# Performance work log

Hardware: AMD Instinct MI355X
Metric: run time of the kernel (lower is better)

Reference implementation:

```python
import jax, jax.numpy as jnp
import numpy as np

N_EMBD = 1024
N_HEAD = 16
HEAD_DIM = N_EMBD // N_HEAD
B, T = 2, 2048


def setup_inputs() -> dict:
    key = jax.random.key(0)
    ks = jax.random.split(key, 12)
    s = 0.02
    inp = {
        "x": jax.random.normal(ks[0], (B, T, N_EMBD), dtype=jnp.float32),
        "ln1_g": jnp.ones((N_EMBD,), jnp.float32),
        "ln1_b": jnp.zeros((N_EMBD,), jnp.float32),
        "ln2_g": jnp.ones((N_EMBD,), jnp.float32),
        "ln2_b": jnp.zeros((N_EMBD,), jnp.float32),
        "W_qkv": jax.random.normal(ks[1], (N_EMBD, 3 * N_EMBD), jnp.float32) * s,
        "b_qkv": jnp.zeros((3 * N_EMBD,), jnp.float32),
        "W_o": jax.random.normal(ks[2], (N_EMBD, N_EMBD), jnp.float32) * s,
        "b_o": jnp.zeros((N_EMBD,), jnp.float32),
        "W_fc": jax.random.normal(ks[3], (N_EMBD, 4 * N_EMBD), jnp.float32) * s,
        "b_fc": jnp.zeros((4 * N_EMBD,), jnp.float32),
        "W_proj": jax.random.normal(ks[4], (4 * N_EMBD, N_EMBD), jnp.float32) * s,
        "b_proj": jnp.zeros((N_EMBD,), jnp.float32),
    }
    return inp


def _layernorm(x, g, b, eps=1e-5):
    mu = jnp.mean(x, axis=-1, keepdims=True)
    var = jnp.var(x, axis=-1, keepdims=True)
    return (x - mu) * jax.lax.rsqrt(var + eps) * g + b


def _block(x, ln1_g, ln1_b, ln2_g, ln2_b, W_qkv, b_qkv, W_o, b_o, W_fc, b_fc, W_proj, b_proj):
    # --- attention sub-block (pre-LN) ---
    h = _layernorm(x, ln1_g, ln1_b)
    qkv = h @ W_qkv + b_qkv                     # [B,T,3E]
    q, k, v = jnp.split(qkv, 3, axis=-1)
    def split_heads(t):
        return t.reshape(B, T, N_HEAD, HEAD_DIM).transpose(0, 2, 1, 3)  # [B,H,T,D]
    q, k, v = split_heads(q), split_heads(k), split_heads(v)
    scores = jnp.einsum("bhqd,bhkd->bhqk", q, k) / (HEAD_DIM ** 0.5)
    causal = jnp.tril(jnp.ones((T, T), dtype=bool))
    scores = jnp.where(causal, scores, jnp.float32(-jnp.inf))
    probs = jax.nn.softmax(scores, axis=-1)
    attn = jnp.einsum("bhqk,bhkd->bhqd", probs, v)        # [B,H,T,D]
    attn = attn.transpose(0, 2, 1, 3).reshape(B, T, N_EMBD)
    x = x + attn @ W_o + b_o
    # --- MLP sub-block (pre-LN) ---
    h = _layernorm(x, ln2_g, ln2_b)
    h = jax.nn.gelu(h @ W_fc + b_fc, approximate=False)
    x = x + h @ W_proj + b_proj
    return x


def reference(x, ln1_g, ln1_b, ln2_g, ln2_b, W_qkv, b_qkv, W_o, b_o, W_fc, b_fc, W_proj, b_proj):
    return _block(x, ln1_g, ln1_b, ln2_g, ln2_b, W_qkv, b_qkv, W_o, b_o, W_fc, b_fc, W_proj, b_proj)
```

## Files before the change

kernel.cpp:

```cpp
#include <hip/hip_runtime.h>
#include <hip/hip_bf16.h>


#define TT 2048
#define EE 1024
#define NH 16
#define HD 64

#define AS1 __attribute__((address_space(1)))
#define AS3 __attribute__((address_space(3)))

using bf16x8 = __bf16 __attribute__((ext_vector_type(8)));
using bf16x4 = __bf16 __attribute__((ext_vector_type(4)));
using f32x4  = float __attribute__((ext_vector_type(4)));

__global__ __launch_bounds__(256) void convt_kernel(const float* __restrict__ W,
                                                    __bf16* __restrict__ WT,
                                                    int K, int N) {
    __shared__ __bf16 t[32][33];
    int n0 = blockIdx.x * 32, k0 = blockIdx.y * 32;
    int tid = threadIdx.x;
    int r = tid >> 3, c4 = (tid & 7) * 4;
    float4 v = *(const float4*)(W + (size_t)(k0 + r) * N + n0 + c4);
    t[r][c4 + 0] = (__bf16)v.x; t[r][c4 + 1] = (__bf16)v.y;
    t[r][c4 + 2] = (__bf16)v.z; t[r][c4 + 3] = (__bf16)v.w;
    __syncthreads();
    bf16x4 o;
    o[0] = t[c4 + 0][r]; o[1] = t[c4 + 1][r];
    o[2] = t[c4 + 2][r]; o[3] = t[c4 + 3][r];
    *(bf16x4*)(WT + (size_t)(n0 + r) * K + k0 + c4) = o;
}

__global__ __launch_bounds__(256) void ln_kernel(const float* __restrict__ x,
                                                 const float* __restrict__ g,
                                                 const float* __restrict__ bta,
                                                 __bf16* __restrict__ out) {
    int row = blockIdx.x;
    int tid = threadIdx.x;
    const float4 xv = *(const float4*)(x + (size_t)row * EE + tid * 4);
    float s  = xv.x + xv.y + xv.z + xv.w;
    float ss = xv.x*xv.x + xv.y*xv.y + xv.z*xv.z + xv.w*xv.w;
    __shared__ float rs[256], rss[256];
    rs[tid] = s; rss[tid] = ss;
    __syncthreads();
    for (int st = 128; st > 0; st >>= 1) {
        if (tid < st) { rs[tid] += rs[tid+st]; rss[tid] += rss[tid+st]; }
        __syncthreads();
    }
    float mean = rs[0] * (1.0f / EE);
    float var  = rss[0] * (1.0f / EE) - mean * mean;
    float rstd = rsqrtf(var + 1e-5f);
    const float4 gv = *(const float4*)(g + tid * 4);
    const float4 bv = *(const float4*)(bta + tid * 4);
    bf16x4 ov;
    ov[0] = (__bf16)((xv.x - mean) * rstd * gv.x + bv.x);
    ov[1] = (__bf16)((xv.y - mean) * rstd * gv.y + bv.y);
    ov[2] = (__bf16)((xv.z - mean) * rstd * gv.z + bv.z);
    ov[3] = (__bf16)((xv.w - mean) * rstd * gv.w + bv.w);
    *(bf16x4*)(out + (size_t)row * EE + tid * 4) = ov;
}

template<int TM, int TN, bool GELU, bool RESID, bool QKV, typename CT>
__global__ __launch_bounds__(256) void gemm_bt_kernel(const __bf16* __restrict__ A,
                                                      const __bf16* __restrict__ BT,
                                                      const float* __restrict__ bias,
                                                      const float* resid, CT* C,
                                                      __bf16* vT,
                                                      int M, int N, int K) {
    constexpr int MT = TM / 32;
    constexpr int NT = TN / 32;
    __shared__ __align__(16) __bf16 As[TM][32];
    __shared__ __align__(16) __bf16 Bs[TN][32];
    int tid = threadIdx.x, wave = tid >> 6, lane = tid & 63;
    int quad = lane >> 4, l16 = lane & 15;
    int wm = wave >> 1, wn = wave & 1;
    int m0 = blockIdx.y * TM, n0 = blockIdx.x * TN;

    f32x4 acc[MT][NT] = {};

    int srow = wave * 16 + (lane >> 2);
    int scol = (lane & 3) * 8;

    for (int kb = 0; kb < K; kb += 32) {
#pragma unroll
        for (int p = 0; p < TM / 64; p++) {
            const __bf16* g = A + (size_t)(m0 + p * 64 + srow) * K + kb + scol;
            __builtin_amdgcn_global_load_lds((AS1 const void*)g,
                                             (AS3 void*)&As[p * 64 + wave * 16][0], 16, 0, 0);
        }
#pragma unroll
        for (int p = 0; p < TN / 64; p++) {
            const __bf16* g = BT + (size_t)(n0 + p * 64 + srow) * K + kb + scol;
            __builtin_amdgcn_global_load_lds((AS1 const void*)g,
                                             (AS3 void*)&Bs[p * 64 + wave * 16][0], 16, 0, 0);
        }
        __syncthreads();
        bf16x8 af[MT], bfr[NT];
#pragma unroll
        for (int mt = 0; mt < MT; mt++)
            af[mt] = *(const bf16x8*)(&As[wm * (MT * 16) + mt * 16 + l16][quad * 8]);
#pragma unroll
        for (int nt = 0; nt < NT; nt++)
            bfr[nt] = *(const bf16x8*)(&Bs[wn * (NT * 16) + nt * 16 + l16][quad * 8]);
#pragma unroll
        for (int mt = 0; mt < MT; mt++)
#pragma unroll
            for (int nt = 0; nt < NT; nt++)
                acc[mt][nt] = __builtin_amdgcn_mfma_f32_16x16x32_bf16(af[mt], bfr[nt],
                                                                      acc[mt][nt], 0, 0, 0);
        __syncthreads();
    }

#pragma unroll
    for (int nt = 0; nt < NT; nt++) {
        int c = n0 + wn * (NT * 16) + nt * 16 + l16;
        float bv = bias[c];
#pragma unroll
        for (int mt = 0; mt < MT; mt++) {
#pragma unroll
            for (int r = 0; r < 4; r++) {
                int row = m0 + wm * (MT * 16) + mt * 16 + quad * 4 + r;
                float v = acc[mt][nt][r] + bv;
                if (GELU)  v = 0.5f * v * (1.0f + erff(v * 0.70710678118f));
                if (RESID) v += resid[(size_t)row * N + c];
                if (!QKV) {
                    C[(size_t)row * N + c] = (CT)v;
                } else {
                    if (c < 2 * EE) {
                        ((__bf16*)C)[(size_t)row * (2 * EE) + c] = (__bf16)v;
                    } else {
                        int cv = c - 2 * EE;
                        int bb = row >> 11, t = row & (TT - 1);
                        vT[((size_t)(bb * NH + (cv >> 6)) * HD + (cv & 63)) * TT + t] =
                            (__bf16)v;
                    }
                }
            }
        }
    }
}

__global__ __launch_bounds__(256) void flash_attn_kernel(const __bf16* __restrict__ qkv,
                                                         const __bf16* __restrict__ vT,
                                                         __bf16* __restrict__ out) {
    int h = blockIdx.y, b = blockIdx.z;
    int tid = threadIdx.x, wave = tid >> 6, lane = tid & 63;
    int quad = lane >> 4, l16 = lane & 15;

    __shared__ __align__(16) __bf16 Ks[128 * 72];
    __shared__ __align__(16) __bf16 Ps[4][16 * 136];

    size_t base = (size_t)b * TT * (2 * EE);

    int srow = tid >> 3;
    int scol = (tid & 7) * 8;
    const __bf16* kbase  = qkv + base + EE + h * HD + scol;
    const __bf16* vrow = vT + (size_t)(b * NH + h) * HD * TT + (size_t)l16 * TT + quad * 8;
    __bf16* Psw = &Ps[wave][0];

    int nTiles = (int)gridDim.x * 2;

    for (int pass = 0; pass < 2; pass++) {
        int qt = pass == 0 ? (nTiles - 1 - blockIdx.x) : blockIdx.x;
        int q0 = qt * 64;

        int qrow = q0 + wave * 16 + l16;
        const __bf16* qp = qkv + base + (size_t)qrow * (2 * EE) + h * HD;
        bf16x8 aq0 = *(const bf16x8*)(qp + quad * 8);
        bf16x8 aq1 = *(const bf16x8*)(qp + 32 + quad * 8);

        f32x4 oacc[4] = {};
        float lsum[4] = {0.f, 0.f, 0.f, 0.f};
        int qg_base = q0 + wave * 16 + quad * 4;

        int nIter = (qt >> 1) + 1;

        bf16x8 kr[4];
#pragma unroll
        for (int p = 0; p < 4; p++)
            kr[p] = *(const bf16x8*)(kbase + (size_t)(32 * p + srow) * (2 * EE));

        for (int kt = 0; kt < nIter; ++kt) {
            int k0 = kt * 128;
#pragma unroll
            for (int p = 0; p < 4; p++)
                *(bf16x8*)(&Ks[(32 * p + srow) * 72 + scol]) = kr[p];
            __syncthreads();

            bf16x8 vf[4][4];
#pragma unroll
            for (int dt = 0; dt < 4; dt++)
#pragma unroll
                for (int w = 0; w < 4; w++)
                    vf[dt][w] = *(const bf16x8*)(vrow + (size_t)dt * (16 * TT) + k0 + w * 32);

            if (kt < nIter - 1) {
                int kn = k0 + 128;
#pragma unroll
                for (int p = 0; p < 4; p++)
                    kr[p] = *(const bf16x8*)(kbase + (size_t)(kn + 32 * p + srow) * (2 * EE));
            }

            f32x4 s[8];
#pragma unroll
            for (int nt = 0; nt < 8; nt++) {
                bf16x8 bk0 = *(const bf16x8*)(&Ks[(nt * 16 + l16) * 72 + quad * 8]);
                bf16x8 bk1 = *(const bf16x8*)(&Ks[(nt * 16 + l16) * 72 + 32 + quad * 8]);
                f32x4 z = {};
                z = __builtin_amdgcn_mfma_f32_16x16x32_bf16(aq0, bk0, z, 0, 0, 0);
                s[nt] = __builtin_amdgcn_mfma_f32_16x16x32_bf16(aq1, bk1, z, 0, 0, 0);
            }

            bool maskt = (kt == nIter - 1);
#pragma unroll
            for (int nt = 0; nt < 8; nt++) {
                int key = k0 + nt * 16 + l16;
                int cb = 2 * nt + (l16 >> 3);
#pragma unroll
                for (int r = 0; r < 4; r++) {
                    float p;
                    if (maskt && key > qg_base + r) p = 0.0f;
                    else p = __expf(fminf(s[nt][r] * 0.125f, 30.0f));
                    lsum[r] += p;
                    int q = quad * 4 + r;
                    int col = (((cb & 8) | ((cb - 2 * q) & 7)) << 3) | (l16 & 7);
                    Psw[q * 136 + col] = (__bf16)p;
                }
            }

#pragma unroll
            for (int w = 0; w < 4; w++) {
                int cbr = 4 * w + quad;
                int colr = ((cbr & 8) | ((cbr - 2 * l16) & 7)) << 3;
                bf16x8 ap = *(const bf16x8*)(&Psw[l16 * 136 + colr]);
#pragma unroll
                for (int dt = 0; dt < 4; dt++)
                    oacc[dt] = __builtin_amdgcn_mfma_f32_16x16x32_bf16(ap, vf[dt][w],
                                                                       oacc[dt], 0, 0, 0);
            }
            __syncthreads();
        }

#pragma unroll
        for (int off = 1; off < 16; off <<= 1)
#pragma unroll
            for (int r = 0; r < 4; r++) lsum[r] += __shfl_xor(lsum[r], off);
#pragma unroll
        for (int dt = 0; dt < 4; dt++) {
#pragma unroll
            for (int r = 0; r < 4; r++) {
                int qg = qg_base + r;
                out[((size_t)b * TT + qg) * EE + h * HD + dt * 16 + l16] =
                    (__bf16)(oacc[dt][r] / lsum[r]);
            }
        }
    }
}

extern "C" void kernel_launch(void* const* d_in, const int* in_sizes, int n_in,
                              void* d_out, int out_size, void* d_ws, size_t ws_size,
                              hipStream_t stream) {
    const float* x     = (const float*)d_in[0];
    const float* ln1g  = (const float*)d_in[1];
    const float* ln1b  = (const float*)d_in[2];
    const float* ln2g  = (const float*)d_in[3];
    const float* ln2b  = (const float*)d_in[4];
    const float* Wqkv  = (const float*)d_in[5];
    const float* bqkv  = (const float*)d_in[6];
    const float* Wo    = (const float*)d_in[7];
    const float* bo    = (const float*)d_in[8];
    const float* Wfc   = (const float*)d_in[9];
    const float* bfc   = (const float*)d_in[10];
    const float* Wproj = (const float*)d_in[11];
    const float* bproj = (const float*)d_in[12];
    float* out = (float*)d_out;

    const int M = 2 * TT;

    __bf16* ws = (__bf16*)d_ws;
    __bf16* regQ   = ws;
    __bf16* regS   = ws + 16777216;
    __bf16* WfcT   = ws + 20971520;
    __bf16* qkv    = regQ;
    __bf16* vT     = regQ + 8388608;
    __bf16* WqkvT  = regQ + 12582912;
    __bf16* WoT    = regQ + 15728640;
    __bf16* ff     = regQ;
    __bf16* h1 = regS, *atn = regS, *h2 = regS;
    __bf16* WprojT = regS;
    float*  x1 = out;

    convt_kernel<<<dim3(3 * EE / 32, EE / 32), 256, 0, stream>>>(Wqkv, WqkvT, EE, 3 * EE);
    convt_kernel<<<dim3(EE / 32, EE / 32), 256, 0, stream>>>(Wo, WoT, EE, EE);
    convt_kernel<<<dim3(4 * EE / 32, EE / 32), 256, 0, stream>>>(Wfc, WfcT, EE, 4 * EE);

    ln_kernel<<<M, 256, 0, stream>>>(x, ln1g, ln1b, h1);
    gemm_bt_kernel<128, 128, false, false, true, __bf16>
        <<<dim3(3 * EE / 128, M / 128), 256, 0, stream>>>(
        h1, WqkvT, bqkv, nullptr, qkv, vT, M, 3 * EE, EE);
    flash_attn_kernel<<<dim3(TT / 128, NH, 2), 256, 0, stream>>>(qkv, vT, atn);
    gemm_bt_kernel<128, 64, false, true, false, float>
        <<<dim3(EE / 64, M / 128), 256, 0, stream>>>(
        atn, WoT, bo, x, x1, nullptr, M, EE, EE);
    ln_kernel<<<M, 256, 0, stream>>>(x1, ln2g, ln2b, h2);
    gemm_bt_kernel<128, 128, true, false, false, __bf16>
        <<<dim3(4 * EE / 128, M / 128), 256, 0, stream>>>(
        h2, WfcT, bfc, nullptr, ff, nullptr, M, 4 * EE, EE);
    convt_kernel<<<dim3(EE / 32, 4 * EE / 32), 256, 0, stream>>>(Wproj, WprojT, 4 * EE, EE);
    gemm_bt_kernel<128, 64, false, true, false, float>
        <<<dim3(EE / 64, M / 128), 256, 0, stream>>>(
        ff, WprojT, bproj, x1, out, nullptr, M, EE, 4 * EE);
}
```

Baseline: 443.6 us.

## Triple-buffer GEMM LDS tiles with async prefetch and use fast GELU approximation

```diff
diff --git a/kernel.cpp b/kernel.cpp
--- a/kernel.cpp
+++ b/kernel.cpp
@@ -13,6 +13,28 @@
 using bf16x8 = __bf16 __attribute__((ext_vector_type(8)));
 using bf16x4 = __bf16 __attribute__((ext_vector_type(4)));
 using f32x4  = float __attribute__((ext_vector_type(4)));
+
+template<int N> __device__ __forceinline__ void vm_wait() {
+    if constexpr (N == 0)      asm volatile("s_waitcnt vmcnt(0)" ::: "memory");
+    else if constexpr (N == 3) asm volatile("s_waitcnt vmcnt(3)" ::: "memory");
+    else                       asm volatile("s_waitcnt vmcnt(4)" ::: "memory");
+}
+
+__device__ __forceinline__ float gelu_fast(float v) {
+    float z  = v * 0.70710678118f;
+    float az = fabsf(z);
+    float t  = __builtin_amdgcn_rcpf(__builtin_fmaf(0.3275911f, az, 1.0f));
+    float p  = t * __builtin_fmaf(t,
+                   __builtin_fmaf(t,
+                     __builtin_fmaf(t,
+                       __builtin_fmaf(t, 1.061405429f, -1.453152027f),
+                       1.421413741f),
+                     -0.284496736f),
+                   0.254829592f);
+    float e  = __expf(-az * az);
+    float er = copysignf(1.0f - p * e, z);
+    return 0.5f * v * (1.0f + er);
+}
 
 __global__ __launch_bounds__(256) void convt_kernel(const float* __restrict__ W,
                                                     __bf16* __restrict__ WT,
@@ -69,8 +91,9 @@
                                                       int M, int N, int K) {
     constexpr int MT = TM / 32;
     constexpr int NT = TN / 32;
-    __shared__ __align__(16) __bf16 As[TM][32];
-    __shared__ __align__(16) __bf16 Bs[TN][32];
+    constexpr int LOADS = TM / 64 + TN / 64;
+    __shared__ __align__(16) __bf16 As[3][TM][32];
+    __shared__ __align__(16) __bf16 Bs[3][TN][32];
     int tid = threadIdx.x, wave = tid >> 6, lane = tid & 63;
     int quad = lane >> 4, l16 = lane & 15;
     int wm = wave >> 1, wn = wave & 1;
@@ -81,34 +104,52 @@
     int srow = wave * 16 + (lane >> 2);
     int scol = (lane & 3) * 8;
 
-    for (int kb = 0; kb < K; kb += 32) {
+    auto STAGE = [&](int buf, int kt) {
+        int kb = kt << 5;
 #pragma unroll
         for (int p = 0; p < TM / 64; p++) {
             const __bf16* g = A + (size_t)(m0 + p * 64 + srow) * K + kb + scol;
             __builtin_amdgcn_global_load_lds((AS1 const void*)g,
-                                             (AS3 void*)&As[p * 64 + wave * 16][0], 16, 0, 0);
+                                             (AS3 void*)&As[buf][p * 64 + wave * 16][0],
+                                             16, 0, 0);
         }
 #pragma unroll
         for (int p = 0; p < TN / 64; p++) {
             const __bf16* g = BT + (size_t)(n0 + p * 64 + srow) * K + kb + scol;
             __builtin_amdgcn_global_load_lds((AS1 const void*)g,
-                                             (AS3 void*)&Bs[p * 64 + wave * 16][0], 16, 0, 0);
-        }
-        __syncthreads();
+                                             (AS3 void*)&Bs[buf][p * 64 + wave * 16][0],
+                                             16, 0, 0);
+        }
+    };
+
+    const int nk = K >> 5;
+    STAGE(0, 0);
+    STAGE(1, 1);
+    vm_wait<LOADS>();
+    __builtin_amdgcn_s_barrier();
+
+    for (int t = 0; t < nk; ++t) {
+        const int cur = t % 3;
+        if (t + 2 < nk) STAGE((t + 2) % 3, t + 2);
+
         bf16x8 af[MT], bfr[NT];
 #pragma unroll
         for (int mt = 0; mt < MT; mt++)
-            af[mt] = *(const bf16x8*)(&As[wm * (MT * 16) + mt * 16 + l16][quad * 8]);
+            af[mt] = *(const bf16x8*)(&As[cur][wm * (MT * 16) + mt * 16 + l16][quad * 8]);
 #pragma unroll
         for (int nt = 0; nt < NT; nt++)
-            bfr[nt] = *(const bf16x8*)(&Bs[wn * (NT * 16) + nt * 16 + l16][quad * 8]);
+            bfr[nt] = *(const bf16x8*)(&Bs[cur][wn * (NT * 16) + nt * 16 + l16][quad * 8]);
 #pragma unroll
         for (int mt = 0; mt < MT; mt++)
 #pragma unroll
             for (int nt = 0; nt < NT; nt++)
                 acc[mt][nt] = __builtin_amdgcn_mfma_f32_16x16x32_bf16(af[mt], bfr[nt],
                                                                       acc[mt][nt], 0, 0, 0);
-        __syncthreads();
+        if (t + 1 < nk) {
+            if (t + 2 < nk) vm_wait<LOADS>();
+            else            vm_wait<0>();
+            __builtin_amdgcn_s_barrier();
+        }
     }
 
 #pragma unroll
@@ -121,7 +162,7 @@
             for (int r = 0; r < 4; r++) {
                 int row = m0 + wm * (MT * 16) + mt * 16 + quad * 4 + r;
                 float v = acc[mt][nt][r] + bv;
-                if (GELU)  v = 0.5f * v * (1.0f + erff(v * 0.70710678118f));
+                if (GELU)  v = gelu_fast(v);
                 if (RESID) v += resid[(size_t)row * N + c];
                 if (!QKV) {
                     C[(size_t)row * N + c] = (CT)v;
```

After: 429.3 us. 3.2% less time.
